# Optimization experiments

Measured on AMD Instinct MI355X. Metric: run time of the kernel, lower is better.

Reference implementation:

```python
import jax, jax.numpy as jnp
import numpy as np

IN_C = 256
GROUPS = 32
ED = 256  # ResnetBlock embed_dim
EPS = 1e-5
B, L = 16, 2048


def setup_inputs() -> dict:
    key = jax.random.key(0)
    ks = jax.random.split(key, 8)

    def rn(k, shape, s=0.05):
        return jax.random.normal(k, shape, dtype=jnp.float32) * s

    d = {
        "x": jax.random.normal(ks[0], (B, IN_C, L), dtype=jnp.float32),
        "t": jax.random.normal(ks[1], (B, 256, 1), dtype=jnp.float32),
    }
    i = 2
    for p in ["r1", "r2"]:
        d[f"{p}_gn1_w"] = jnp.ones((IN_C,), jnp.float32)
        d[f"{p}_gn1_b"] = jnp.zeros((IN_C,), jnp.float32)
        d[f"{p}_c1_w"] = rn(ks[i], (ED, IN_C, 3)); i += 1
        d[f"{p}_c1_b"] = jnp.zeros((ED,), jnp.float32)
        d[f"{p}_gn2_w"] = jnp.ones((ED,), jnp.float32)
        d[f"{p}_gn2_b"] = jnp.zeros((ED,), jnp.float32)
        d[f"{p}_c2_w"] = rn(ks[i], (IN_C, ED, 3)); i += 1
        d[f"{p}_c2_b"] = jnp.zeros((IN_C,), jnp.float32)
    d["lin_w"] = rn(ks[i], (3 * IN_C, IN_C, 1))
    d["lin_b"] = jnp.zeros((3 * IN_C,), jnp.float32)
    return d


def _gn(x, w, b):
    # GroupNorm over (C//G, L) per group, affine per-channel
    Bx, C, Lx = x.shape
    xr = x.reshape(Bx, GROUPS, -1)
    m = xr.mean(-1, keepdims=True)
    v = xr.var(-1, keepdims=True)
    xr = (xr - m) * jax.lax.rsqrt(v + EPS)
    return xr.reshape(Bx, C, Lx) * w[None, :, None] + b[None, :, None]


def _conv(x, w, b, pad):
    y = jax.lax.conv_general_dilated(
        x, w, window_strides=(1,), padding=[(pad, pad)],
        dimension_numbers=("NCH", "OIH", "NCH"))
    return y + b[None, :, None]


def _res(x, t, gn1w, gn1b, c1w, c1b, gn2w, gn2b, c2w, c2b):
    h = _conv(jax.nn.relu(_gn(x, gn1w, gn1b)), c1w, c1b, 1) + t
    h = _conv(jax.nn.relu(_gn(h, gn2w, gn2b)), c2w, c2b, 1)
    return x + h


def reference(x, t,
              r1_gn1_w, r1_gn1_b, r1_c1_w, r1_c1_b, r1_gn2_w, r1_gn2_b, r1_c2_w, r1_c2_b,
              r2_gn1_w, r2_gn1_b, r2_c1_w, r2_c1_b, r2_gn2_w, r2_gn2_b, r2_c2_w, r2_c2_b,
              lin_w, lin_b):
    x = _res(x, t, r1_gn1_w, r1_gn1_b, r1_c1_w, r1_c1_b, r1_gn2_w, r1_gn2_b, r1_c2_w, r1_c2_b)
    kqv = _conv(x, lin_w, lin_b, 0)                      # (B, 3C, L)
    kt, qt, vt = jnp.split(kqv, 3, axis=1)               # each (B, C, L)
    scale = 1.0 / np.sqrt(x.shape[1]).astype(np.float32)
    scores = jnp.einsum("bcq,bck->bqk", qt, kt) * scale  # (B, L, L)
    attn = jax.nn.softmax(scores, axis=2)
    av = jnp.einsum("bqk,bck->bcq", attn, vt)            # (B, C, L)
    return _res(av, t, r2_gn1_w, r2_gn1_b, r2_c1_w, r2_c1_b, r2_gn2_w, r2_gn2_b, r2_c2_w, r2_c2_b)
```

## Files before the change

kernel.cpp:

```cpp
#include <hip/hip_runtime.h>

typedef unsigned short u16;
typedef unsigned int u32;
typedef __attribute__((ext_vector_type(8))) short bf16x8;
typedef __attribute__((ext_vector_type(4))) float f32x4;
typedef __attribute__((ext_vector_type(16))) float f32x16;

#define NB 16
#define NC 256
#define NL 2048
#define EPS 1e-5f
#define QSC2 0.0901684401f
#define DEFER 11.54f
#define TROWS 2050
#define PHALF ((size_t)NB * NC * NL)

__device__ __forceinline__ float bf2f(u16 a) {
  union { unsigned u; float f; } v; v.u = (unsigned)a << 16; return v.f;
}
__device__ __forceinline__ u16 f2bf(float f) {
  union { float f; unsigned u; } v; v.f = f;
  return (u16)((v.u + 0x7fffu + ((v.u >> 16) & 1u)) >> 16);
}
__device__ __forceinline__ u32 cvtpk(float lo, float hi) {
  u32 r;
  asm("v_cvt_pk_bf16_f32 %0, %1, %2" : "=v"(r) : "v"(lo), "v"(hi));
  return r;
}
__device__ __forceinline__ float ex2(float x) {
  float r;
  asm("v_exp_f32 %0, %1" : "=v"(r) : "v"(x));
  return r;
}
__device__ __forceinline__ void gld16(const void* gsrc, void* ldst) {
  __builtin_amdgcn_global_load_lds(
      (const __attribute__((address_space(1))) void*)gsrc,
      (__attribute__((address_space(3))) void*)ldst, 16, 0, 0);
}

__global__ __launch_bounds__(256)
void pack_w(const float* __restrict__ w1, const float* __restrict__ w2,
            const float* __restrict__ w3, const float* __restrict__ w4,
            const float* __restrict__ lw, const float* __restrict__ lb,
            u16* __restrict__ Wp, u16* __restrict__ Wq, float* __restrict__ bq)
{
  const int a = blockIdx.y;
  const int gid = blockIdx.x * 256 + threadIdx.x;
  if (a < 4) {
    const float* w = a == 0 ? w1 : a == 1 ? w2 : a == 2 ? w3 : w4;
    const int d = gid >> 16, rem = gid & 65535;
    const int oc = rem >> 8, ic = rem & 255;
    Wp[a * 196608 + gid] = f2bf(w[(oc * 256 + ic) * 3 + d]);
  } else {
    const int oc = gid >> 8;
    const float s = (oc >= 256 && oc < 512) ? QSC2 : 1.0f;
    Wq[gid] = f2bf(lw[gid] * s);
    if (gid < 768) bq[gid] = lb[gid] * ((gid >= 256 && gid < 512) ? QSC2 : 1.0f);
  }
}

__global__ __launch_bounds__(256)
void stats_f32(const float* __restrict__ x, float2* __restrict__ pstat)
{
  const int blk = blockIdx.x;
  const float* p = x + (size_t)blk * NL + threadIdx.x * 8;
  const float4 a = ((const float4*)p)[0];
  const float4 c4 = ((const float4*)p)[1];
  float s = (a.x + a.y) + (a.z + a.w) + (c4.x + c4.y) + (c4.z + c4.w);
  float ss = a.x*a.x + a.y*a.y + a.z*a.z + a.w*a.w + c4.x*c4.x + c4.y*c4.y + c4.z*c4.z + c4.w*c4.w;
#pragma unroll
  for (int o = 32; o > 0; o >>= 1) { s += __shfl_down(s, o); ss += __shfl_down(ss, o); }
  __shared__ float2 red[4];
  if ((threadIdx.x & 63) == 0) red[threadIdx.x >> 6] = make_float2(s, ss);
  __syncthreads();
  if (threadIdx.x == 0)
    pstat[blk] = make_float2(red[0].x + red[1].x + red[2].x + red[3].x,
                             red[0].y + red[1].y + red[2].y + red[3].y);
}

__global__ __launch_bounds__(256)
void apply_f32T(const float* __restrict__ x, const float2* __restrict__ pstat,
                const float* __restrict__ gw, const float* __restrict__ gb,
                u16* __restrict__ outT)
{
  __shared__ float2 chs[256];
  __shared__ float gm[32], gi[32];
  __shared__ float ta[32][257];
  const int t = threadIdx.x, b = blockIdx.y;
  const int L0 = blockIdx.x * 32;
  chs[t] = pstat[b * 256 + t];
  __syncthreads();
  if (t < 32) {
    float S = 0.f, SS = 0.f;
#pragma unroll
    for (int j = 0; j < 8; ++j) { S += chs[t * 8 + j].x; SS += chs[t * 8 + j].y; }
    const float mean = S * (1.f / 16384.f);
    const float var = SS * (1.f / 16384.f) - mean * mean;
    gm[t] = mean; gi[t] = rsqrtf(var + EPS);
  }
  {
    const int cR = t >> 3, lq = (t & 7) * 4;
#pragma unroll
    for (int i = 0; i < 8; ++i) {
      const int c = i * 32 + cR;
      const float4 v = *(const float4*)&x[((size_t)b * NC + c) * NL + L0 + lq];
      ta[lq + 0][c] = v.x; ta[lq + 1][c] = v.y; ta[lq + 2][c] = v.z; ta[lq + 3][c] = v.w;
    }
  }
  __syncthreads();
  const int g = t & 31, rbase = t >> 5;
  float ga[8], be[8];
#pragma unroll
  for (int j = 0; j < 4; ++j)
#pragma unroll
    for (int k = 0; k < 2; ++k) {
      const int c = 2 * g + 64 * j + k;
      const int grp = c >> 3;
      ga[j * 2 + k] = gw[c] * gi[grp];
      be[j * 2 + k] = gb[c] - gm[grp] * ga[j * 2 + k];
    }
#pragma unroll
  for (int ri = 0; ri < 4; ++ri) {
    const int row = rbase + ri * 8;
    u16* orow = outT + ((size_t)b * TROWS + 1 + L0 + row) * 256;
#pragma unroll
    for (int j = 0; j < 4; ++j) {
      const int c = 2 * g + 64 * j;
      const float v0 = ta[row][c], v1 = ta[row][c + 1];
      ushort2 o;
      o.x = f2bf(fmaxf(fmaf(v0, ga[j * 2], be[j * 2]), 0.f));
      o.y = f2bf(fmaxf(fmaf(v1, ga[j * 2 + 1], be[j * 2 + 1]), 0.f));
      *(ushort2*)(orow + c) = o;
    }
  }
  if (blockIdx.x == 0 && t < 128) {
    const int r = (t >> 6) ? 2049 : 0;
    *(ushort4*)(outT + ((size_t)b * TROWS + r) * 256 + (t & 63) * 4) = (ushort4){0, 0, 0, 0};
  }
}

__global__ __launch_bounds__(256)
void apply_TT(const u16* __restrict__ inT, const float2* __restrict__ pstat,
              const float* __restrict__ gw, const float* __restrict__ gb,
              u16* __restrict__ outT)
{
  __shared__ float2 chs[256];
  __shared__ float gm[32], gi[32];
  const int t = threadIdx.x, b = blockIdx.y;
  {
    float S = 0.f, SS = 0.f;
#pragma unroll
    for (int p = 0; p < 16; ++p) {
      const float2 v = pstat[((size_t)b * 16 + p) * 256 + t];
      S += v.x; SS += v.y;
    }
    chs[t] = make_float2(S, SS);
  }
  __syncthreads();
  if (t < 32) {
    float S = 0.f, SS = 0.f;
#pragma unroll
    for (int j = 0; j < 8; ++j) { S += chs[t * 8 + j].x; SS += chs[t * 8 + j].y; }
    const float mean = S * (1.f / 16384.f);
    const float var = SS * (1.f / 16384.f) - mean * mean;
    gm[t] = mean; gi[t] = rsqrtf(var + EPS);
  }
  __syncthreads();
  const int g = t & 31;
  float ga[8], be[8];
#pragma unroll
  for (int j = 0; j < 8; ++j) {
    ga[j] = gw[g * 8 + j] * gi[g];
    be[j] = gb[g * 8 + j] - gm[g] * ga[j];
  }
#pragma unroll
  for (int j = 0; j < 16; ++j) {
    const int row = blockIdx.x * 128 + j * 8 + (t >> 5);
    const size_t off = ((size_t)b * TROWS + 1 + row) * 256 + g * 8;
    const bf16x8 h = *(const bf16x8*)(inT + off);
    u16 o[8];
#pragma unroll
    for (int i = 0; i < 8; ++i)
      o[i] = f2bf(fmaxf(fmaf(bf2f(((const u16*)&h)[i]), ga[i], be[i]), 0.f));
    *(bf16x8*)(outT + off) = *(bf16x8*)o;
  }
  if (blockIdx.x == 0 && t < 128) {
    const int r = (t >> 6) ? 2049 : 0;
    *(ushort4*)(outT + ((size_t)b * TROWS + r) * 256 + (t & 63) * 4) = (ushort4){0, 0, 0, 0};
  }
}

template<int OCT, int KD, bool HAS_T, int RESM, bool STATS>
__global__ __launch_bounds__(256, 2)
void conv_mfma(const u16* __restrict__ xT, const u16* __restrict__ Wp,
               const float* __restrict__ bias, const float* __restrict__ tadd,
               u16* __restrict__ outT, u16* __restrict__ vTout,
               const float* __restrict__ resf, float* __restrict__ outf,
               float2* __restrict__ pstatOut)
{
  constexpr int DOFF = (KD == 3) ? 0 : 1;
  __shared__ __align__(16) u16 xs[2][130 * 128];
  const int lb = blockIdx.x * 128;
  const int ocb = blockIdx.y * 128;
  const int b = blockIdx.z;
  const int tid = threadIdx.x;
  const int w = tid >> 6, lane = tid & 63;
  const int l15 = lane & 15, lg = lane >> 4;
  const int woc = (w >> 1) * 64, wl = (w & 1) * 64;

  f32x4 acc[4][4];
#pragma unroll
  for (int i = 0; i < 4; ++i)
#pragma unroll
    for (int j = 0; j < 4; ++j) acc[i][j] = (f32x4){0.f, 0.f, 0.f, 0.f};

  const u16* xTb = xT + ((size_t)b * TROWS + lb) * 256;

  auto stageX = [&](int buf, int ich) {
    u16* xb = &xs[buf][0];
#pragma unroll
    for (int j = 0; j < 8; ++j) {
      const int slot = w * 512 + j * 64 + lane;
      const int row = slot >> 4, g0 = slot & 15;
      const int g = (g0 & 8) | ((g0 ^ row) & 7);
      gld16(xTb + (size_t)row * 256 + ich * 128 + g * 8, xb + (size_t)(w * 512 + j * 64) * 8);
    }
    if (w == 0 && lane < 32) {
      const int slot = 2048 + lane;
      const int row = slot >> 4, g0 = slot & 15;
      const int g = (g0 & 8) | ((g0 ^ row) & 7);
      gld16(xTb + (size_t)row * 256 + ich * 128 + g * 8, xb + (size_t)2048 * 8);
    }
  };
  auto loadW = [&](bf16x8 (&af)[KD][4], int p) {
    const int ich = p >> 2, kc = p & 3;
#pragma unroll
    for (int d = 0; d < KD; ++d)
#pragma unroll
      for (int mf = 0; mf < 4; ++mf)
        af[d][mf] = *(const bf16x8*)(Wp + ((size_t)d * OCT + ocb + woc + mf * 16 + l15) * 256
                                        + ich * 128 + kc * 32 + lg * 8);
  };

  bf16x8 afbuf[2][KD][4];
  stageX(0, 0);
  loadW(afbuf[0], 0);
  __syncthreads();
  stageX(1, 1);

#pragma unroll
  for (int p = 0; p < 8; ++p) {
    if (p == 4) __syncthreads();
    if (p < 7) loadW(afbuf[(p + 1) & 1], p + 1);
    const int kc = p & 3;
    const int gg = kc * 4 + lg;
    const char* xb = (const char*)&xs[p >> 2][0];
#pragma unroll
    for (int nf = 0; nf < 4; ++nf) {
#pragma unroll
      for (int d = 0; d < KD; ++d) {
        const int r = wl + nf * 16 + l15 + d + DOFF;
        const int gsr = (gg & 8) | ((gg ^ r) & 7);
        const bf16x8 bf = *(const bf16x8*)(xb + r * 256 + gsr * 16);
#pragma unroll
        for (int mf = 0; mf < 4; ++mf)
          acc[mf][nf] = __builtin_amdgcn_mfma_f32_16x16x32_bf16(afbuf[p & 1][d][mf], bf, acc[mf][nf], 0, 0, 0);
      }
    }
  }

  if (OCT == 768 && ocb >= 512) {
    __syncthreads();
    u16* tile = (u16*)&xs[0][0];
#pragma unroll
    for (int mf = 0; mf < 4; ++mf) {
      const int cl = woc + mf * 16 + lg * 4;
      const float4 bv = *(const float4*)&bias[ocb + cl];
#pragma unroll
      for (int nf = 0; nf < 4; ++nf) {
        const int ll = wl + nf * 16 + l15;
        const f32x4 a = acc[mf][nf];
        tile[(cl + 0) * 136 + ll] = f2bf(a[0] + bv.x);
        tile[(cl + 1) * 136 + ll] = f2bf(a[1] + bv.y);
        tile[(cl + 2) * 136 + ll] = f2bf(a[2] + bv.z);
        tile[(cl + 3) * 136 + ll] = f2bf(a[3] + bv.w);
      }
    }
    __syncthreads();
    const int cv0 = ocb - 512;
#pragma unroll
    for (int it = 0; it < 8; ++it) {
      const int chunk = it * 256 + tid;
      const int row = chunk >> 4, off = (chunk & 15) * 8;
      const bf16x8 v = *(const bf16x8*)&tile[row * 136 + off];
      *(bf16x8*)(vTout + ((size_t)b * NC + cv0 + row) * NL + lb + off) = v;
    }
    return;
  }

  float cs[4][4], cq[4][4];
  if (STATS) {
#pragma unroll
    for (int i = 0; i < 4; ++i)
#pragma unroll
      for (int j = 0; j < 4; ++j) { cs[i][j] = 0.f; cq[i][j] = 0.f; }
  }

#pragma unroll
  for (int mf = 0; mf < 4; ++mf) {
    const int ocbase = ocb + woc + mf * 16 + lg * 4;
    float4 bv = *(const float4*)&bias[ocbase];
    if (HAS_T) {
      const float4 tv = *(const float4*)&tadd[b * 256 + ocbase];
      bv.x += tv.x; bv.y += tv.y; bv.z += tv.z; bv.w += tv.w;
    }
#pragma unroll
    for (int nf = 0; nf < 4; ++nf) {
      const int l = lb + wl + nf * 16 + l15;
      const f32x4 a = acc[mf][nf];
      float v0 = a[0] + bv.x, v1 = a[1] + bv.y, v2 = a[2] + bv.z, v3 = a[3] + bv.w;
      if (RESM >= 1) {
        const float* rp = resf + ((size_t)b * NC + ocbase) * NL + l;
        v0 += rp[0]; v1 += rp[NL]; v2 += rp[2 * (size_t)NL]; v3 += rp[3 * (size_t)NL];
      }
      if (STATS) {
        cs[mf][0] += v0; cq[mf][0] += v0 * v0;
        cs[mf][1] += v1; cq[mf][1] += v1 * v1;
        cs[mf][2] += v2; cq[mf][2] += v2 * v2;
        cs[mf][3] += v3; cq[mf][3] += v3 * v3;
      }
      if (RESM == 2) {
        float* op = outf + ((size_t)b * NC + ocbase) * NL + l;
        op[0] = v0; op[NL] = v1; op[2 * (size_t)NL] = v2; op[3 * (size_t)NL] = v3;
      } else if (OCT == 256) {
        ushort4 st = {f2bf(v0), f2bf(v1), f2bf(v2), f2bf(v3)};
        *(ushort4*)(outT + ((size_t)b * TROWS + 1 + l) * 256 + ocbase) = st;
      } else {
        ushort4 st = {f2bf(v0), f2bf(v1), f2bf(v2), f2bf(v3)};
        *(ushort4*)(outT + ((size_t)b * NL + l) * 512 + ocbase) = st;
      }
    }
  }

  if (STATS) {
    __syncthreads();
    float* sred = (float*)&xs[0][0];
#pragma unroll
    for (int mf = 0; mf < 4; ++mf)
#pragma unroll
      for (int j = 0; j < 4; ++j) {
        float s = cs[mf][j], q = cq[mf][j];
#pragma unroll
        for (int m = 1; m < 16; m <<= 1) { s += __shfl_xor(s, m); q += __shfl_xor(q, m); }
        if (l15 == 0) {
          const int cl = woc + mf * 16 + lg * 4 + j;
          sred[(w & 1) * 128 + cl] = s;
          sred[256 + (w & 1) * 128 + cl] = q;
        }
      }
    __syncthreads();
    if (tid < 128) {
      const float s = sred[tid] + sred[128 + tid];
      const float q = sred[256 + tid] + sred[384 + tid];
      pstatOut[((size_t)b * 16 + blockIdx.x) * 256 + ocb + tid] = make_float2(s, q);
    }
  }
}

#define AKVB 32
#define ATILES 32

__global__ __launch_bounds__(256, 2)
void attn_mfma(const u16* __restrict__ kq, const u16* __restrict__ vT,
               u16* __restrict__ part, float2* __restrict__ stats)
{
  __shared__ u16 ks[2][32 * 256];
  __shared__ u16 vs[2][256 * 32];

  const int fid = blockIdx.x;
  const int xcd = fid & 7, idx = fid >> 3;
  const int b = (xcd << 1) | (idx & 1);
  const int rest = idx >> 1;
  const int qt = rest & 15, half = rest >> 4;
  const int kvbase = half * 1024;

  const int tid = threadIdx.x;
  const int w = tid >> 6, lane = tid & 63;
  const int l31 = lane & 31, lh = lane >> 5;
  const int q = qt * 128 + w * 32 + l31;

  const u16* kqb = kq + (size_t)b * NL * 512;
  const u16* vb  = vT + (size_t)b * NC * NL;

  auto stage = [&](int buf, int kv0) {
#pragma unroll
    for (int j = 0; j < 4; ++j) {
      const int slot = w * 256 + j * 64 + lane;
      const int r = slot >> 5, c = slot & 31;
      const int g = (c - r) & 31;
      gld16(kqb + (size_t)(kv0 + r) * 512 + g * 8, &ks[buf][(size_t)(w * 256 + j * 64) * 8]);
    }
#pragma unroll
    for (int j = 0; j < 4; ++j) {
      const int slot = w * 256 + j * 64 + lane;
      const int r = slot >> 2, c = slot & 3;
      const int g = (c - r - (r >> 2)) & 3;
      gld16(vb + (size_t)r * NL + kv0 + g * 8, &vs[buf][(size_t)(w * 256 + j * 64) * 8]);
    }
  };

  bf16x8 qf[16];
  {
    const u16* qp = kqb + (size_t)q * 512 + 256 + lh * 8;
#pragma unroll
    for (int kk = 0; kk < 16; ++kk) qf[kk] = *(const bf16x8*)(qp + kk * 16);
  }

  f32x16 o[8];
#pragma unroll
  for (int i = 0; i < 8; ++i)
    o[i] = (f32x16){0.f,0.f,0.f,0.f,0.f,0.f,0.f,0.f,0.f,0.f,0.f,0.f,0.f,0.f,0.f,0.f};
  float m = -1e30f, lsum = 0.f;

  stage(0, kvbase);
  __syncthreads();

  for (int t = 0; t < ATILES; ++t) {
    const int cur = t & 1;
    if (t + 1 < ATILES) stage(cur ^ 1, kvbase + (t + 1) * AKVB);
    const u16* kbase = &ks[cur][0];
    f32x16 s = (f32x16){0.f,0.f,0.f,0.f,0.f,0.f,0.f,0.f,0.f,0.f,0.f,0.f,0.f,0.f,0.f,0.f};
#pragma unroll
    for (int kk = 0; kk < 16; ++kk) {
      const int gn = 2 * kk + lh;
      const bf16x8 kf = *(const bf16x8*)(kbase + (l31 * 32 + ((gn + l31) & 31)) * 8);
      s = __builtin_amdgcn_mfma_f32_32x32x16_bf16(kf, qf[kk], s, 0, 0, 0);
    }
    float tm = s[0];
#pragma unroll
    for (int i = 1; i < 16; ++i) tm = fmaxf(tm, s[i]);
    tm = fmaxf(tm, __shfl_xor(tm, 32));
    if (!__all(tm <= m + DEFER)) {
      const float mn = fmaxf(m, tm);
      const float corr = ex2(m - mn);
      m = mn; lsum *= corr;
#pragma unroll
      for (int i = 0; i < 8; ++i) o[i] *= corr;
    }
    float sum = 0.f;
#pragma unroll
    for (int i = 0; i < 16; ++i) { s[i] = ex2(s[i] - m); sum += s[i]; }
    sum += __shfl_xor(sum, 32);
    lsum += sum;
    u32 pk[8];
#pragma unroll
    for (int i = 0; i < 8; ++i) pk[i] = cvtpk(s[2 * i], s[2 * i + 1]);
    const u16* vbase = &vs[cur][0];
#pragma unroll
    for (int ksx = 0; ksx < 2; ++ksx) {
      const int base = ksx * 4;
      const u32 send0 = lh ? pk[base + 0] : pk[base + 2];
      const u32 send1 = lh ? pk[base + 1] : pk[base + 3];
      const u32 r0 = (u32)__shfl_xor((int)send0, 32);
      const u32 r1 = (u32)__shfl_xor((int)send1, 32);
      union { u32 wd[4]; bf16x8 v; } pu;
      pu.wd[0] = lh ? r0 : pk[base + 0];
      pu.wd[1] = lh ? r1 : pk[base + 1];
      pu.wd[2] = lh ? pk[base + 2] : r0;
      pu.wd[3] = lh ? pk[base + 3] : r1;
      const bf16x8 pf = pu.v;
      const int gn = 2 * ksx + lh;
#pragma unroll
      for (int mf = 0; mf < 8; ++mf) {
        const int row = mf * 32 + l31;
        const bf16x8 vf = *(const bf16x8*)(vbase + (row * 4 + ((gn + row + (row >> 2)) & 3)) * 8);
        o[mf] = __builtin_amdgcn_mfma_f32_32x32x16_bf16(vf, pf, o[mf], 0, 0, 0);
      }
    }
    if (t + 1 < ATILES) __syncthreads();
  }
  u16* pp = part + half * PHALF + (size_t)b * NC * NL + q;
#pragma unroll
  for (int mf = 0; mf < 8; ++mf)
#pragma unroll
    for (int r = 0; r < 16; ++r) {
      const int c = mf * 32 + (r & 3) + 8 * (r >> 2) + 4 * lh;
      pp[(size_t)c * NL] = f2bf(o[mf][r]);
    }
  if (lane < 32)
    stats[((size_t)half * NB + b) * NL + q] = make_float2(m, lsum);
}

__global__ __launch_bounds__(256)
void attn_combine(const u16* __restrict__ part, const float2* __restrict__ stats,
                  float* __restrict__ av, float2* __restrict__ pstat)
{
  const int c = blockIdx.x, b = blockIdx.y;
  const int l0 = threadIdx.x * 8;
  const u16* p0 = part + ((size_t)b * NC + c) * NL + l0;
  const u16* p1 = p0 + PHALF;
  const float2* s0p = stats + (size_t)b * NL + l0;
  const float2* s1p = stats + ((size_t)NB + b) * NL + l0;
  const bf16x8 P0 = *(const bf16x8*)p0;
  const bf16x8 P1 = *(const bf16x8*)p1;
  float* op = av + ((size_t)b * NC + c) * NL + l0;
  float s = 0.f, ss = 0.f;
  float res[8];
#pragma unroll
  for (int j = 0; j < 8; ++j) {
    const float2 a = s0p[j], bb = s1p[j];
    const float M = fmaxf(a.x, bb.x);
    const float e0 = ex2(a.x - M), e1 = ex2(bb.x - M);
    const float den = 1.f / (a.y * e0 + bb.y * e1);
    const float r = (bf2f(((const u16*)&P0)[j]) * e0 + bf2f(((const u16*)&P1)[j]) * e1) * den;
    res[j] = r;
    s += r; ss += r * r;
  }
  *(float4*)op = make_float4(res[0], res[1], res[2], res[3]);
  *(float4*)(op + 4) = make_float4(res[4], res[5], res[6], res[7]);
#pragma unroll
  for (int o = 32; o > 0; o >>= 1) { s += __shfl_down(s, o); ss += __shfl_down(ss, o); }
  __shared__ float2 red[4];
  if ((threadIdx.x & 63) == 0) red[threadIdx.x >> 6] = make_float2(s, ss);
  __syncthreads();
  if (threadIdx.x == 0)
    pstat[b * 256 + c] = make_float2(red[0].x + red[1].x + red[2].x + red[3].x,
                                     red[0].y + red[1].y + red[2].y + red[3].y);
}

extern "C" void kernel_launch(void* const* d_in, const int* in_sizes, int n_in,
                              void* d_out, int out_size, void* d_ws, size_t ws_size,
                              hipStream_t stream)
{
  (void)in_sizes; (void)n_in; (void)out_size; (void)ws_size;
  const float* x        = (const float*)d_in[0];
  const float* t        = (const float*)d_in[1];
  const float* r1_gn1_w = (const float*)d_in[2];
  const float* r1_gn1_b = (const float*)d_in[3];
  const float* r1_c1_w  = (const float*)d_in[4];
  const float* r1_c1_b  = (const float*)d_in[5];
  const float* r1_gn2_w = (const float*)d_in[6];
  const float* r1_gn2_b = (const float*)d_in[7];
  const float* r1_c2_w  = (const float*)d_in[8];
  const float* r1_c2_b  = (const float*)d_in[9];
  const float* r2_gn1_w = (const float*)d_in[10];
  const float* r2_gn1_b = (const float*)d_in[11];
  const float* r2_c1_w  = (const float*)d_in[12];
  const float* r2_c1_b  = (const float*)d_in[13];
  const float* r2_gn2_w = (const float*)d_in[14];
  const float* r2_gn2_b = (const float*)d_in[15];
  const float* r2_c2_w  = (const float*)d_in[16];
  const float* r2_c2_b  = (const float*)d_in[17];
  const float* lin_w    = (const float*)d_in[18];
  const float* lin_b    = (const float*)d_in[19];

  float* out = (float*)d_out;

  const size_t TSZ = (size_t)NB * TROWS * 256 * 2;
  u16* tA  = (u16*)d_ws;
  u16* tB  = (u16*)((char*)d_ws + TSZ);
  u16* kq  = tB;
  float* avF = (float*)((char*)d_ws + TSZ);
  u16* tC  = (u16*)((char*)d_ws + 3 * TSZ);
  u16* vT  = tC;
  u16* Wp  = (u16*)((char*)d_ws + 4 * TSZ);
  u16* Wq  = Wp + 4 * 196608;
  float* bq = (float*)(Wq + 196608);
  float2* pstat = (float2*)((char*)bq + 4096);

  const dim3 gPack(768, 5);
  const dim3 gC(16, 2, NB);
  const dim3 gQ(16, 6, NB);
  const dim3 gS16(16, NB);
  const dim3 gA64(64, NB);
  const dim3 gCmb(NC, NB);

  pack_w<<<gPack, 256, 0, stream>>>(r1_c1_w, r1_c2_w, r2_c1_w, r2_c2_w, lin_w, lin_b, Wp, Wq, bq);

  stats_f32<<<NB * NC, 256, 0, stream>>>(x, pstat);
  apply_f32T<<<gA64, 256, 0, stream>>>(x, pstat, r1_gn1_w, r1_gn1_b, tA);
  conv_mfma<256, 3, true, 0, true><<<gC, 256, 0, stream>>>(tA, Wp, r1_c1_b, t, tB, nullptr, nullptr, nullptr, pstat);
  apply_TT<<<gS16, 256, 0, stream>>>(tB, pstat, r1_gn2_w, r1_gn2_b, tC);
  conv_mfma<256, 3, false, 1, false><<<gC, 256, 0, stream>>>(tC, Wp + 196608, r1_c2_b, nullptr, tA, nullptr, x, nullptr, nullptr);

  conv_mfma<768, 1, false, 0, false><<<gQ, 256, 0, stream>>>(tA, Wq, bq, nullptr, kq, vT, nullptr, nullptr, nullptr);
  attn_mfma<<<512, 256, 0, stream>>>(kq, vT, (u16*)out, (float2*)tA);
  attn_combine<<<gCmb, 256, 0, stream>>>((const u16*)out, (const float2*)tA, avF, pstat);

  apply_f32T<<<gA64, 256, 0, stream>>>(avF, pstat, r2_gn1_w, r2_gn1_b, tA);
  conv_mfma<256, 3, true, 0, true><<<gC, 256, 0, stream>>>(tA, Wp + 2 * 196608, r2_c1_b, t, tC, nullptr, nullptr, nullptr, pstat);
  apply_TT<<<gS16, 256, 0, stream>>>(tC, pstat, r2_gn2_w, r2_gn2_b, tA);
  conv_mfma<256, 3, false, 2, false><<<gC, 256, 0, stream>>>(tA, Wp + 3 * 196608, r2_c2_b, nullptr, nullptr, nullptr, avF, out, nullptr);
}
```

Baseline: 357.2 us.

## Emit attention output in bf16 transposed layout and reuse staged X across output-channel tiles

attn_combine now writes the attention result directly as a bf16 transposed, padded buffer with per-chunk partial stats. This replaces the fp32 av tensor, so the second resblock can use apply_TT instead of apply_f32T and read its residual as bf16. The conv kernel switches to a 1D grid with swizzled block IDs. For the QKV projection, one block now computes two 128-channel output tiles from the same staged input, which cuts redundant input loads. The trade-off is lower residual precision (bf16) and fewer blocks for the QKV conv.

Measured after the change: 359.0 us. No clear change (+0.5%).

```diff
diff --git a/kernel.cpp b/kernel.cpp
--- a/kernel.cpp
+++ b/kernel.cpp
@@ -195,24 +195,29 @@
 void conv_mfma(const u16* __restrict__ xT, const u16* __restrict__ Wp,
                const float* __restrict__ bias, const float* __restrict__ tadd,
                u16* __restrict__ outT, u16* __restrict__ vTout,
-               const float* __restrict__ resf, float* __restrict__ outf,
-               float2* __restrict__ pstatOut)
+               const float* __restrict__ resf, const u16* __restrict__ resT,
+               float* __restrict__ outf, float2* __restrict__ pstatOut)
 {
   constexpr int DOFF = (KD == 3) ? 0 : 1;
   __shared__ __align__(16) u16 xs[2][130 * 128];
-  const int lb = blockIdx.x * 128;
-  const int ocb = blockIdx.y * 128;
+  const int bx = blockIdx.x;
   const int b = blockIdx.z;
+  int lbx, ocb0, nsub;
+  if (OCT == 256) {
+    const int wid = (bx & 7) * 4 + (bx >> 3);
+    lbx = wid >> 1; ocb0 = (wid & 1) * 128; nsub = 1;
+  } else {
+    const int wid = (bx & 7) * 8 + (bx >> 3);
+    const int yy = wid & 3;
+    lbx = wid >> 2;
+    if (yy < 2) { ocb0 = yy * 256; nsub = 2; }
+    else { ocb0 = 512 + (yy - 2) * 128; nsub = 1; }
+  }
+  const int lb = lbx * 128;
   const int tid = threadIdx.x;
   const int w = tid >> 6, lane = tid & 63;
   const int l15 = lane & 15, lg = lane >> 4;
   const int woc = (w >> 1) * 64, wl = (w & 1) * 64;
-
-  f32x4 acc[4][4];
-#pragma unroll
-  for (int i = 0; i < 4; ++i)
-#pragma unroll
-    for (int j = 0; j < 4; ++j) acc[i][j] = (f32x4){0.f, 0.f, 0.f, 0.f};
 
   const u16* xTb = xT + ((size_t)b * TROWS + lb) * 256;
 
@@ -232,7 +237,7 @@
       gld16(xTb + (size_t)row * 256 + ich * 128 + g * 8, xb + (size_t)2048 * 8);
     }
   };
-  auto loadW = [&](bf16x8 (&af)[KD][4], int p) {
+  auto loadW = [&](bf16x8 (&af)[KD][4], int p, int ocb) {
     const int ich = p >> 2, kc = p & 3;
 #pragma unroll
     for (int d = 0; d < KD; ++d)
@@ -242,127 +247,141 @@
                                         + ich * 128 + kc * 32 + lg * 8);
   };
 
-  bf16x8 afbuf[2][KD][4];
   stageX(0, 0);
-  loadW(afbuf[0], 0);
   __syncthreads();
   stageX(1, 1);
 
-#pragma unroll
-  for (int p = 0; p < 8; ++p) {
-    if (p == 4) __syncthreads();
-    if (p < 7) loadW(afbuf[(p + 1) & 1], p + 1);
-    const int kc = p & 3;
-    const int gg = kc * 4 + lg;
-    const char* xb = (const char*)&xs[p >> 2][0];
-#pragma unroll
-    for (int nf = 0; nf < 4; ++nf) {
-#pragma unroll
-      for (int d = 0; d < KD; ++d) {
-        const int r = wl + nf * 16 + l15 + d + DOFF;
-        const int gsr = (gg & 8) | ((gg ^ r) & 7);
-        const bf16x8 bf = *(const bf16x8*)(xb + r * 256 + gsr * 16);
-#pragma unroll
-        for (int mf = 0; mf < 4; ++mf)
-          acc[mf][nf] = __builtin_amdgcn_mfma_f32_16x16x32_bf16(afbuf[p & 1][d][mf], bf, acc[mf][nf], 0, 0, 0);
-      }
-    }
-  }
-
-  if (OCT == 768 && ocb >= 512) {
-    __syncthreads();
-    u16* tile = (u16*)&xs[0][0];
-#pragma unroll
-    for (int mf = 0; mf < 4; ++mf) {
-      const int cl = woc + mf * 16 + lg * 4;
-      const float4 bv = *(const float4*)&bias[ocb + cl];
+  for (int sidx = 0; sidx < nsub; ++sidx) {
+    const int ocb = ocb0 + sidx * 128;
+    f32x4 acc[4][4];
+#pragma unroll
+    for (int i = 0; i < 4; ++i)
+#pragma unroll
+      for (int j = 0; j < 4; ++j) acc[i][j] = (f32x4){0.f, 0.f, 0.f, 0.f};
+
+    bf16x8 afbuf[2][KD][4];
+    loadW(afbuf[0], 0, ocb);
+
+#pragma unroll
+    for (int p = 0; p < 8; ++p) {
+      if (p == 4 && sidx == 0) __syncthreads();
+      if (p < 7) loadW(afbuf[(p + 1) & 1], p + 1, ocb);
+      const int kc = p & 3;
+      const int gg = kc * 4 + lg;
+      const char* xb = (const char*)&xs[p >> 2][0];
 #pragma unroll
       for (int nf = 0; nf < 4; ++nf) {
-        const int ll = wl + nf * 16 + l15;
-        const f32x4 a = acc[mf][nf];
-        tile[(cl + 0) * 136 + ll] = f2bf(a[0] + bv.x);
-        tile[(cl + 1) * 136 + ll] = f2bf(a[1] + bv.y);
-        tile[(cl + 2) * 136 + ll] = f2bf(a[2] + bv.z);
-        tile[(cl + 3) * 136 + ll] = f2bf(a[3] + bv.w);
-      }
-    }
-    __syncthreads();
-    const int cv0 = ocb - 512;
-#pragma unroll
-    for (int it = 0; it < 8; ++it) {
-      const int chunk = it * 256 + tid;
-      const int row = chunk >> 4, off = (chunk & 15) * 8;
-      const bf16x8 v = *(const bf16x8*)&tile[row * 136 + off];
-      *(bf16x8*)(vTout + ((size_t)b * NC + cv0 + row) * NL + lb + off) = v;
-    }
-    return;
-  }
-
-  float cs[4][4], cq[4][4];
-  if (STATS) {
-#pragma unroll
-    for (int i = 0; i < 4; ++i)
-#pragma unroll
-      for (int j = 0; j < 4; ++j) { cs[i][j] = 0.f; cq[i][j] = 0.f; }
-  }
-
-#pragma unroll
-  for (int mf = 0; mf < 4; ++mf) {
-    const int ocbase = ocb + woc + mf * 16 + lg * 4;
-    float4 bv = *(const float4*)&bias[ocbase];
-    if (HAS_T) {
-      const float4 tv = *(const float4*)&tadd[b * 256 + ocbase];
-      bv.x += tv.x; bv.y += tv.y; bv.z += tv.z; bv.w += tv.w;
-    }
-#pragma unroll
-    for (int nf = 0; nf < 4; ++nf) {
-      const int l = lb + wl + nf * 16 + l15;
-      const f32x4 a = acc[mf][nf];
-      float v0 = a[0] + bv.x, v1 = a[1] + bv.y, v2 = a[2] + bv.z, v3 = a[3] + bv.w;
-      if (RESM >= 1) {
-        const float* rp = resf + ((size_t)b * NC + ocbase) * NL + l;
-        v0 += rp[0]; v1 += rp[NL]; v2 += rp[2 * (size_t)NL]; v3 += rp[3 * (size_t)NL];
-      }
-      if (STATS) {
-        cs[mf][0] += v0; cq[mf][0] += v0 * v0;
-        cs[mf][1] += v1; cq[mf][1] += v1 * v1;
-        cs[mf][2] += v2; cq[mf][2] += v2 * v2;
-        cs[mf][3] += v3; cq[mf][3] += v3 * v3;
-      }
-      if (RESM == 2) {
-        float* op = outf + ((size_t)b * NC + ocbase) * NL + l;
-        op[0] = v0; op[NL] = v1; op[2 * (size_t)NL] = v2; op[3 * (size_t)NL] = v3;
-      } else if (OCT == 256) {
-        ushort4 st = {f2bf(v0), f2bf(v1), f2bf(v2), f2bf(v3)};
-        *(ushort4*)(outT + ((size_t)b * TROWS + 1 + l) * 256 + ocbase) = st;
-      } else {
-        ushort4 st = {f2bf(v0), f2bf(v1), f2bf(v2), f2bf(v3)};
-        *(ushort4*)(outT + ((size_t)b * NL + l) * 512 + ocbase) = st;
-      }
-    }
-  }
-
-  if (STATS) {
-    __syncthreads();
-    float* sred = (float*)&xs[0][0];
-#pragma unroll
-    for (int mf = 0; mf < 4; ++mf)
-#pragma unroll
-      for (int j = 0; j < 4; ++j) {
-        float s = cs[mf][j], q = cq[mf][j];
-#pragma unroll
-        for (int m = 1; m < 16; m <<= 1) { s += __shfl_xor(s, m); q += __shfl_xor(q, m); }
-        if (l15 == 0) {
-          const int cl = woc + mf * 16 + lg * 4 + j;
-          sred[(w & 1) * 128 + cl] = s;
-          sred[256 + (w & 1) * 128 + cl] = q;
+#pragma unroll
+        for (int d = 0; d < KD; ++d) {
+          const int r = wl + nf * 16 + l15 + d + DOFF;
+          const int gsr = (gg & 8) | ((gg ^ r) & 7);
+          const bf16x8 bf = *(const bf16x8*)(xb + r * 256 + gsr * 16);
+#pragma unroll
+          for (int mf = 0; mf < 4; ++mf)
+            acc[mf][nf] = __builtin_amdgcn_mfma_f32_16x16x32_bf16(afbuf[p & 1][d][mf], bf, acc[mf][nf], 0, 0, 0);
         }
       }
-    __syncthreads();
-    if (tid < 128) {
-      const float s = sred[tid] + sred[128 + tid];
-      const float q = sred[256 + tid] + sred[384 + tid];
-      pstatOut[((size_t)b * 16 + blockIdx.x) * 256 + ocb + tid] = make_float2(s, q);
+    }
+
+    if (OCT == 768 && ocb0 >= 512) {
+      __syncthreads();
+      u16* tile = (u16*)&xs[0][0];
+#pragma unroll
+      for (int mf = 0; mf < 4; ++mf) {
+        const int cl = woc + mf * 16 + lg * 4;
+        const float4 bv = *(const float4*)&bias[ocb + cl];
+#pragma unroll
+        for (int nf = 0; nf < 4; ++nf) {
+          const int ll = wl + nf * 16 + l15;
+          const f32x4 a = acc[mf][nf];
+          tile[(cl + 0) * 136 + ll] = f2bf(a[0] + bv.x);
+          tile[(cl + 1) * 136 + ll] = f2bf(a[1] + bv.y);
+          tile[(cl + 2) * 136 + ll] = f2bf(a[2] + bv.z);
+          tile[(cl + 3) * 136 + ll] = f2bf(a[3] + bv.w);
+        }
+      }
+      __syncthreads();
+      const int cv0 = ocb - 512;
+#pragma unroll
+      for (int it = 0; it < 8; ++it) {
+        const int chunk = it * 256 + tid;
+        const int row = chunk >> 4, off = (chunk & 15) * 8;
+        const bf16x8 v = *(const bf16x8*)&tile[row * 136 + off];
+        *(bf16x8*)(vTout + ((size_t)b * NC + cv0 + row) * NL + lb + off) = v;
+      }
+      return;
+    }
+
+    float cs[4][4], cq[4][4];
+    if (STATS) {
+#pragma unroll
+      for (int i = 0; i < 4; ++i)
+#pragma unroll
+        for (int j = 0; j < 4; ++j) { cs[i][j] = 0.f; cq[i][j] = 0.f; }
+    }
+
+#pragma unroll
+    for (int mf = 0; mf < 4; ++mf) {
+      const int ocbase = ocb + woc + mf * 16 + lg * 4;
+      float4 bv = *(const float4*)&bias[ocbase];
+      if (HAS_T) {
+        const float4 tv = *(const float4*)&tadd[b * 256 + ocbase];
+        bv.x += tv.x; bv.y += tv.y; bv.z += tv.z; bv.w += tv.w;
+      }
+#pragma unroll
+      for (int nf = 0; nf < 4; ++nf) {
+        const int l = lb + wl + nf * 16 + l15;
+        const f32x4 a = acc[mf][nf];
+        float v0 = a[0] + bv.x, v1 = a[1] + bv.y, v2 = a[2] + bv.z, v3 = a[3] + bv.w;
+        if (RESM == 1) {
+          const float* rp = resf + ((size_t)b * NC + ocbase) * NL + l;
+          v0 += rp[0]; v1 += rp[NL]; v2 += rp[2 * (size_t)NL]; v3 += rp[3 * (size_t)NL];
+        }
+        if (RESM == 2) {
+          const ushort4 rv = *(const ushort4*)(resT + ((size_t)b * TROWS + 1 + l) * 256 + ocbase);
+          v0 += bf2f(rv.x); v1 += bf2f(rv.y); v2 += bf2f(rv.z); v3 += bf2f(rv.w);
+        }
+        if (STATS) {
+          cs[mf][0] += v0; cq[mf][0] += v0 * v0;
+          cs[mf][1] += v1; cq[mf][1] += v1 * v1;
+          cs[mf][2] += v2; cq[mf][2] += v2 * v2;
+          cs[mf][3] += v3; cq[mf][3] += v3 * v3;
+        }
+        if (RESM == 2) {
+          float* op = outf + ((size_t)b * NC + ocbase) * NL + l;
+          op[0] = v0; op[NL] = v1; op[2 * (size_t)NL] = v2; op[3 * (size_t)NL] = v3;
+        } else if (OCT == 256) {
+          ushort4 st = {f2bf(v0), f2bf(v1), f2bf(v2), f2bf(v3)};
+          *(ushort4*)(outT + ((size_t)b * TROWS + 1 + l) * 256 + ocbase) = st;
+        } else {
+          ushort4 st = {f2bf(v0), f2bf(v1), f2bf(v2), f2bf(v3)};
+          *(ushort4*)(outT + ((size_t)b * NL + l) * 512 + ocbase) = st;
+        }
+      }
+    }
+
+    if (STATS) {
+      __syncthreads();
+      float* sred = (float*)&xs[0][0];
+#pragma unroll
+      for (int mf = 0; mf < 4; ++mf)
+#pragma unroll
+        for (int j = 0; j < 4; ++j) {
+          float s = cs[mf][j], q = cq[mf][j];
+#pragma unroll
+          for (int m = 1; m < 16; m <<= 1) { s += __shfl_xor(s, m); q += __shfl_xor(q, m); }
+          if (l15 == 0) {
+            const int cl = woc + mf * 16 + lg * 4 + j;
+            sred[(w & 1) * 128 + cl] = s;
+            sred[256 + (w & 1) * 128 + cl] = q;
+          }
+        }
+      __syncthreads();
+      if (tid < 128) {
+        const float s = sred[tid] + sred[128 + tid];
+        const float q = sred[256 + tid] + sred[384 + tid];
+        pstatOut[((size_t)b * 16 + lbx) * 256 + ocb + tid] = make_float2(s, q);
+      }
     }
   }
 }
@@ -493,39 +512,44 @@
 
 __global__ __launch_bounds__(256)
 void attn_combine(const u16* __restrict__ part, const float2* __restrict__ stats,
-                  float* __restrict__ av, float2* __restrict__ pstat)
-{
-  const int c = blockIdx.x, b = blockIdx.y;
-  const int l0 = threadIdx.x * 8;
-  const u16* p0 = part + ((size_t)b * NC + c) * NL + l0;
+                  u16* __restrict__ avT, float2* __restrict__ pstat)
+{
+  __shared__ float2 sst[2][128];
+  __shared__ u16 tile[128][264];
+  const int chunk = blockIdx.x, b = blockIdx.y;
+  const int t = threadIdx.x;
+  const int l0 = chunk * 128;
+  if (t < 128) sst[0][t] = stats[(size_t)b * NL + l0 + t];
+  else sst[1][t - 128] = stats[((size_t)NB + b) * NL + l0 + (t - 128)];
+  __syncthreads();
+  const u16* p0 = part + ((size_t)b * NC + t) * NL + l0;
   const u16* p1 = p0 + PHALF;
-  const float2* s0p = stats + (size_t)b * NL + l0;
-  const float2* s1p = stats + ((size_t)NB + b) * NL + l0;
-  const bf16x8 P0 = *(const bf16x8*)p0;
-  const bf16x8 P1 = *(const bf16x8*)p1;
-  float* op = av + ((size_t)b * NC + c) * NL + l0;
   float s = 0.f, ss = 0.f;
-  float res[8];
-#pragma unroll
-  for (int j = 0; j < 8; ++j) {
-    const float2 a = s0p[j], bb = s1p[j];
-    const float M = fmaxf(a.x, bb.x);
-    const float e0 = ex2(a.x - M), e1 = ex2(bb.x - M);
-    const float den = 1.f / (a.y * e0 + bb.y * e1);
-    const float r = (bf2f(((const u16*)&P0)[j]) * e0 + bf2f(((const u16*)&P1)[j]) * e1) * den;
-    res[j] = r;
-    s += r; ss += r * r;
-  }
-  *(float4*)op = make_float4(res[0], res[1], res[2], res[3]);
-  *(float4*)(op + 4) = make_float4(res[4], res[5], res[6], res[7]);
-#pragma unroll
-  for (int o = 32; o > 0; o >>= 1) { s += __shfl_down(s, o); ss += __shfl_down(ss, o); }
-  __shared__ float2 red[4];
-  if ((threadIdx.x & 63) == 0) red[threadIdx.x >> 6] = make_float2(s, ss);
-  __syncthreads();
-  if (threadIdx.x == 0)
-    pstat[b * 256 + c] = make_float2(red[0].x + red[1].x + red[2].x + red[3].x,
-                                     red[0].y + red[1].y + red[2].y + red[3].y);
+#pragma unroll 4
+  for (int j = 0; j < 16; ++j) {
+    const bf16x8 a8 = *(const bf16x8*)(p0 + j * 8);
+    const bf16x8 b8 = *(const bf16x8*)(p1 + j * 8);
+#pragma unroll
+    for (int k = 0; k < 8; ++k) {
+      const int l = j * 8 + k;
+      const float2 sa = sst[0][l], sb = sst[1][l];
+      const float M = fmaxf(sa.x, sb.x);
+      const float e0 = ex2(sa.x - M), e1 = ex2(sb.x - M);
+      const float den = 1.f / (sa.y * e0 + sb.y * e1);
+      const float r = (bf2f(((const u16*)&a8)[k]) * e0 + bf2f(((const u16*)&b8)[k]) * e1) * den;
+      tile[l][t] = f2bf(r);
+      s += r; ss += r * r;
+    }
+  }
+  pstat[((size_t)b * 16 + chunk) * 256 + t] = make_float2(s, ss);
+  __syncthreads();
+#pragma unroll
+  for (int it = 0; it < 16; ++it) {
+    const int id = it * 256 + t;
+    const int row = id >> 5, ch = id & 31;
+    const bf16x8 v = *(const bf16x8*)&tile[row][ch * 8];
+    *(bf16x8*)(avT + ((size_t)b * TROWS + 1 + l0 + row) * 256 + ch * 8) = v;
+  }
 }
 
 extern "C" void kernel_launch(void* const* d_in, const int* in_sizes, int n_in,
@@ -560,35 +584,35 @@
   u16* tA  = (u16*)d_ws;
   u16* tB  = (u16*)((char*)d_ws + TSZ);
   u16* kq  = tB;
-  float* avF = (float*)((char*)d_ws + TSZ);
   u16* tC  = (u16*)((char*)d_ws + 3 * TSZ);
   u16* vT  = tC;
   u16* Wp  = (u16*)((char*)d_ws + 4 * TSZ);
   u16* Wq  = Wp + 4 * 196608;
   float* bq = (float*)(Wq + 196608);
   float2* pstat = (float2*)((char*)bq + 4096);
+  float2* astat = (float2*)((char*)pstat + 524288);
 
   const dim3 gPack(768, 5);
-  const dim3 gC(16, 2, NB);
-  const dim3 gQ(16, 6, NB);
+  const dim3 gC(32, 1, NB);
+  const dim3 gQ(64, 1, NB);
   const dim3 gS16(16, NB);
   const dim3 gA64(64, NB);
-  const dim3 gCmb(NC, NB);
+  const dim3 gCmb(16, NB);
 
   pack_w<<<gPack, 256, 0, stream>>>(r1_c1_w, r1_c2_w, r2_c1_w, r2_c2_w, lin_w, lin_b, Wp, Wq, bq);
 
   stats_f32<<<NB * NC, 256, 0, stream>>>(x, pstat);
   apply_f32T<<<gA64, 256, 0, stream>>>(x, pstat, r1_gn1_w, r1_gn1_b, tA);
-  conv_mfma<256, 3, true, 0, true><<<gC, 256, 0, stream>>>(tA, Wp, r1_c1_b, t, tB, nullptr, nullptr, nullptr, pstat);
+  conv_mfma<256, 3, true, 0, true><<<gC, 256, 0, stream>>>(tA, Wp, r1_c1_b, t, tB, nullptr, nullptr, nullptr, nullptr, pstat);
   apply_TT<<<gS16, 256, 0, stream>>>(tB, pstat, r1_gn2_w, r1_gn2_b, tC);
-  conv_mfma<256, 3, false, 1, false><<<gC, 256, 0, stream>>>(tC, Wp + 196608, r1_c2_b, nullptr, tA, nullptr, x, nullptr, nullptr);
-
-  conv_mfma<768, 1, false, 0, false><<<gQ, 256, 0, stream>>>(tA, Wq, bq, nullptr, kq, vT, nullptr, nullptr, nullptr);
-  attn_mfma<<<512, 256, 0, stream>>>(kq, vT, (u16*)out, (float2*)tA);
-  attn_combine<<<gCmb, 256, 0, stream>>>((const u16*)out, (const float2*)tA, avF, pstat);
-
-  apply_f32T<<<gA64, 256, 0, stream>>>(avF, pstat, r2_gn1_w, r2_gn1_b, tA);
-  conv_mfma<256, 3, true, 0, true><<<gC, 256, 0, stream>>>(tA, Wp + 2 * 196608, r2_c1_b, t, tC, nullptr, nullptr, nullptr, pstat);
-  apply_TT<<<gS16, 256, 0, stream>>>(tC, pstat, r2_gn2_w, r2_gn2_b, tA);
-  conv_mfma<256, 3, false, 2, false><<<gC, 256, 0, stream>>>(tA, Wp + 3 * 196608, r2_c2_b, nullptr, nullptr, nullptr, avF, out, nullptr);
-}
+  conv_mfma<256, 3, false, 1, false><<<gC, 256, 0, stream>>>(tC, Wp + 196608, r1_c2_b, nullptr, tA, nullptr, x, nullptr, nullptr, nullptr);
+
+  conv_mfma<768, 1, false, 0, false><<<gQ, 256, 0, stream>>>(tA, Wq, bq, nullptr, kq, vT, nullptr, nullptr, nullptr, nullptr);
+  attn_mfma<<<512, 256, 0, stream>>>(kq, vT, (u16*)out, astat);
+  attn_combine<<<gCmb, 256, 0, stream>>>((const u16*)out, astat, tA, pstat);
+
+  apply_TT<<<gS16, 256, 0, stream>>>(tA, pstat, r2_gn1_w, r2_gn1_b, tC);
+  conv_mfma<256, 3, true, 0, true><<<gC, 256, 0, stream>>>(tC, Wp + 2 * 196608, r2_c1_b, t, tB, nullptr, nullptr, nullptr, nullptr, pstat);
+  apply_TT<<<gS16, 256, 0, stream>>>(tB, pstat, r2_gn2_w, r2_gn2_b, tC);
+  conv_mfma<256, 3, false, 2, false><<<gC, 256, 0, stream>>>(tC, Wp + 3 * 196608, r2_c2_b, nullptr, nullptr, nullptr, nullptr, tA, out, nullptr);
+}
```
